# Performance work log

Measured on AMD Instinct MI355X. Metric: run time of the kernel, lower is better.

The kernel has to match this reference:

```python
import jax, jax.numpy as jnp
import numpy as np

N_NODES = 10000
N_EDGES = 160000
T_STEPS = 2
N_SAMPLE = 2
H_DIM = 64
Z_DIM = 32
K_HEADS = 4
N_IN = 4


def setup_inputs() -> dict:
    key = jax.random.key(0)
    ks = jax.random.split(key, 16)
    sc = lambda fan_in: 1.0 / np.sqrt(fan_in).astype(np.float32)
    inp = {}
    inp["inputs"] = jax.random.normal(ks[0], (N_NODES, T_STEPS, N_IN), jnp.float32)
    inp["zA"] = jax.random.normal(ks[1], (N_NODES, N_SAMPLE, Z_DIM), jnp.float32)
    inp["zG"] = jax.random.normal(ks[2], (N_NODES, N_SAMPLE, Z_DIM), jnp.float32)
    inp["src"] = jax.random.randint(ks[3], (N_EDGES,), 0, N_NODES)
    inp["dst"] = jax.random.randint(ks[4], (N_EDGES,), 0, N_NODES)
    # GAT attention projections (K heads, no bias): Linear(z_dim -> h_dim)
    inp["Ws"] = jax.random.normal(ks[5], (K_HEADS, H_DIM, Z_DIM), jnp.float32) * sc(Z_DIM)
    inp["Wd"] = jax.random.normal(ks[6], (K_HEADS, H_DIM, Z_DIM), jnp.float32) * sc(Z_DIM)
    # F2: Linear(2h -> h, no bias), ReLU, Linear(h -> h, no bias)
    inp["F2_w1"] = jax.random.normal(ks[7], (H_DIM, 2 * H_DIM), jnp.float32) * sc(2 * H_DIM)
    inp["F2_w2"] = jax.random.normal(ks[8], (H_DIM, H_DIM), jnp.float32) * sc(H_DIM)
    # F1: Linear(K*h -> h, no bias), ReLU, Linear(h -> h, no bias)
    inp["F1_w1"] = jax.random.normal(ks[9], (H_DIM, K_HEADS * H_DIM), jnp.float32) * sc(K_HEADS * H_DIM)
    inp["F1_w2"] = jax.random.normal(ks[10], (H_DIM, H_DIM), jnp.float32) * sc(H_DIM)
    # x_enc: Linear(n_in -> h) with bias
    inp["xenc_w"] = jax.random.normal(ks[11], (H_DIM, N_IN), jnp.float32) * sc(N_IN)
    inp["xenc_b"] = jnp.zeros((H_DIM,), jnp.float32)
    # out_fc: Linear(h+z -> h), ReLU, Linear(h -> 4)
    inp["out_w1"] = jax.random.normal(ks[12], (H_DIM, H_DIM + Z_DIM), jnp.float32) * sc(H_DIM + Z_DIM)
    inp["out_b1"] = jnp.zeros((H_DIM,), jnp.float32)
    inp["out_w2"] = jax.random.normal(ks[13], (4, H_DIM), jnp.float32) * sc(H_DIM)
    inp["out_b2"] = jnp.zeros((4,), jnp.float32)
    inp["pred_steps"] = 2
    return inp


def reference(inputs, zA, zG, src, dst, Ws, Wd, F2_w1, F2_w2, F1_w1, F1_w2,
              xenc_w, xenc_b, out_w1, out_b1, out_w2, out_b2, pred_steps):
    N, T, _ = inputs.shape
    S = zA.shape[1]
    K = Ws.shape[0]

    # --- edge attention (GAT.attn), computed once per forward ---
    As = jnp.einsum('nsz,khz->nskh', zG, Ws)          # [N, S, K, H]
    Ad = jnp.einsum('nsz,khz->nskh', zG, Wd)
    e = jnp.sum(As[src] * Ad[dst], axis=-1)           # [E, S, K]
    e = jax.nn.leaky_relu(e, 0.01)
    # per-destination softmax over incoming edges (DGL mailbox softmax over dim=1)
    m = jax.ops.segment_max(e, dst, num_segments=N)
    ex = jnp.exp(e - m[dst])
    denom = jax.ops.segment_sum(ex, dst, num_segments=N)
    alpha = ex / denom[dst]                           # [E, S, K]
    deg = jax.ops.segment_sum(jnp.ones((e.shape[0],), e.dtype), dst, num_segments=N)
    deg = jnp.maximum(deg, 1.0)[:, None, None]        # [N, 1, 1]; mean over mailbox dim

    def step(xt):
        xt_enc = xt @ xenc_w.T + xenc_b               # [N, S, H]
        cat = jnp.concatenate([xt_enc[src], xt_enc[dst]], axis=-1)  # [E, S, 2H]
        dA = jax.nn.relu(cat @ F2_w1.T) @ F2_w2.T     # [E, S, H]
        # per-head attention-weighted mean over in-neighbors; loop over K (small, fixed)
        res = [jax.ops.segment_sum(alpha[:, :, k:k + 1] * dA, dst, num_segments=N) / deg
               for k in range(K)]
        res = jnp.concatenate(res, axis=-1)           # [N, S, K*H]
        deltax = jax.nn.relu(res @ F1_w1.T) @ F1_w2.T # [N, S, H]
        h = jnp.concatenate([deltax, zA], axis=-1)    # [N, S, H+Z]
        dx = jax.nn.relu(h @ out_w1.T + out_b1) @ out_w2.T + out_b2  # [N, S, 4]
        return xt + dx

    inp_t = jnp.transpose(inputs, (1, 0, 2))          # [T, N, n_in]
    inp_t = jnp.broadcast_to(inp_t[:, :, None, :], (T, N, S, inp_t.shape[-1]))
    preds = []
    for b in range(0, T, pred_steps):                 # blocks of pred_steps
        xt = inp_t[b]
        for _ in range(pred_steps):
            xt = step(xt)
            preds.append(xt)
    out = jnp.stack(preds, axis=0)                    # [T, N, S, 4]
    return jnp.transpose(out, (1, 0, 2, 3))           # [N, T, S, 4]
```

## Files before the change

### kernel.cpp

```cpp
#include <hip/hip_runtime.h>

#define NN 10000
#define NE 160000
#define TT 2
#define SS 2
#define HH 64
#define ZZ 32
#define KK 4
#define NIN 4

typedef short bf16x8 __attribute__((ext_vector_type(8)));
typedef float f32x4 __attribute__((ext_vector_type(4)));

__device__ __forceinline__ unsigned short f2b(float x) {
    unsigned u = __float_as_uint(x);
    u += 0x7fffu + ((u >> 16) & 1u);
    return (unsigned short)(u >> 16);
}
__device__ __forceinline__ float bf2f(unsigned short u) {
    return __uint_as_float(((unsigned)u) << 16);
}

__device__ __forceinline__ float edge_score(const unsigned* __restrict__ zp,
                                            const float* __restrict__ qf) {
    float a = 0.f;
#pragma unroll
    for (int j = 0; j < 16; ++j) {
        unsigned u = zp[j];
        a += __uint_as_float(u << 16) * qf[2*j]
           + __uint_as_float(u & 0xffff0000u) * qf[2*j+1];
    }
    return a > 0.f ? a : 0.01f*a;
}

__global__ __launch_bounds__(256) void k_prep(
    const float* __restrict__ Ws, const float* __restrict__ Wd,
    const float* __restrict__ F2w1, const float* __restrict__ xw,
    const float* __restrict__ xb, const float* __restrict__ F2w2,
    const float* __restrict__ F1w1, const float* __restrict__ F1w2,
    const float* __restrict__ ow1, const float* __restrict__ ow2,
    const float* __restrict__ zA, const float* __restrict__ zG,
    const float* __restrict__ inputs, const int* __restrict__ dst,
    float* __restrict__ MT, float* __restrict__ G1, float* __restrict__ G2,
    float* __restrict__ c1, float* __restrict__ c2,
    unsigned short* __restrict__ W2b, unsigned short* __restrict__ F1w1b,
    unsigned short* __restrict__ F1w2b, unsigned short* __restrict__ ow1b,
    unsigned short* __restrict__ ow2b, unsigned short* __restrict__ zAb,
    unsigned short* __restrict__ zGb, float* __restrict__ xt,
    int* __restrict__ deg_i)
{
    int b = blockIdx.x;
    int tid = threadIdx.x;
    if (b < 16) {
        int o = b*256 + tid;
        int j = o & 31, i = (o >> 5) & 31, k = o >> 10;
        float acc = 0.0f;
        for (int h = 0; h < HH; ++h)
            acc += Ws[(k*HH + h)*ZZ + i] * Wd[(k*HH + h)*ZZ + j];
        MT[(k*ZZ + j)*ZZ + i] = acc;
    } else if (b == 16) {
        int h = tid >> 2, i = tid & 3;
        float a1 = 0.f, a2 = 0.f;
        for (int j = 0; j < HH; ++j) {
            float x = xw[j*NIN + i];
            a1 += F2w1[h*128 + j] * x;
            a2 += F2w1[h*128 + 64 + j] * x;
        }
        G1[h*4 + i] = a1;
        G2[h*4 + i] = a2;
        if (i == 0) {
            float b1 = 0.f, b2 = 0.f;
            for (int j = 0; j < HH; ++j) {
                float bb = xb[j];
                b1 += F2w1[h*128 + j] * bb;
                b2 += F2w1[h*128 + 64 + j] * bb;
            }
            c1[h] = b1; c2[h] = b2;
        }
    } else {
        int t = (b - 17)*256 + tid;
        if (t < NN*SS*ZZ) { zAb[t] = f2b(zA[t]); zGb[t] = f2b(zG[t]); }
        if (t < HH*HH)    { W2b[t] = f2b(F2w2[t]); F1w2b[t] = f2b(F1w2[t]); }
        if (t < HH*KK*HH) F1w1b[t] = f2b(F1w1[t]);
        if (t < HH*(HH+ZZ)) ow1b[t] = f2b(ow1[t]);
        if (t < 4*HH)     ow2b[t] = f2b(ow2[t]);
        if (t < NN*SS*NIN) {
            int i = t & 3;
            int n = t >> 3;
            xt[t] = inputs[n*(TT*NIN) + i];
        }
        if (t < NE) atomicAdd(deg_i + dst[t], 1);
    }
}

__global__ void k_scan(const int* __restrict__ deg_i, int* __restrict__ offsets,
                       int* __restrict__ cursor) {
    __shared__ int buf0[1024], buf1[1024];
    int tidx = threadIdx.x;
    const int CH = (NN + 1023) / 1024;
    int b0 = tidx * CH;
    int sum = 0;
    for (int i = 0; i < CH; ++i) { int idx = b0 + i; if (idx < NN) sum += deg_i[idx]; }
    buf0[tidx] = sum;
    __syncthreads();
    int* s = buf0; int* d = buf1;
    for (int off = 1; off < 1024; off <<= 1) {
        d[tidx] = s[tidx] + (tidx >= off ? s[tidx - off] : 0);
        __syncthreads();
        int* tmp = s; s = d; d = tmp;
    }
    int run = s[tidx] - sum;
    for (int i = 0; i < CH; ++i) {
        int idx = b0 + i;
        if (idx < NN) { offsets[idx] = run; cursor[idx] = run; run += deg_i[idx]; }
    }
    if (tidx == 0) offsets[NN] = NE;
}

__global__ void k_scatter(const int* __restrict__ src, const int* __restrict__ dst,
                          int* __restrict__ cursor, int* __restrict__ src_by_pos) {
    int e = blockIdx.x * blockDim.x + threadIdx.x;
    if (e >= NE) return;
    int pos = atomicAdd(cursor + dst[e], 1);
    src_by_pos[pos] = src[e];
}

__global__ __launch_bounds__(64) void k_attn_agg0(
    const float* __restrict__ MT, const float* __restrict__ zG,
    const unsigned short* __restrict__ zGb, const int* __restrict__ src_by_pos,
    const int* __restrict__ offsets, const float* __restrict__ xt,
    const float* __restrict__ G1, const float* __restrict__ G2,
    const float* __restrict__ c1, const float* __restrict__ c2,
    float* alpha, unsigned short* __restrict__ agg_b)
{
    __shared__ float sq[128];
    __shared__ float alpha_s[64][4];
    int item = blockIdx.x;
    int n = item >> 1, s = item & 1;
    int l = threadIdx.x;
    int i = l >> 2, k = l & 3;
    int r0 = offsets[n], r1 = offsets[n+1];

    {
        int i0 = l & 31;
        int k0 = l >> 5;
        int k1 = k0 + 2;
        const float* zg = zG + item*ZZ;
        float acc0 = 0.f, acc1 = 0.f;
#pragma unroll
        for (int j = 0; j < ZZ; ++j) {
            float z = zg[j];
            acc0 += MT[(k0*ZZ + j)*ZZ + i0] * z;
            acc1 += MT[(k1*ZZ + j)*ZZ + i0] * z;
        }
        sq[k0*ZZ + i0] = acc0;
        sq[k1*ZZ + i0] = acc1;
    }
    __syncthreads();
    float qf[32];
#pragma unroll
    for (int j = 0; j < 32; ++j) qf[j] = sq[k*ZZ + j];

    float E[8];
    float mx = -1e30f;
    int nit = 0;
    for (int idx = r0 + i; idx < r1; idx += 16, ++nit) {
        int sn = src_by_pos[idx];
        float e = edge_score((const unsigned*)(zGb + (sn*SS + s)*ZZ), qf);
        if (nit < 8) E[nit] = e;
        mx = fmaxf(mx, e);
    }
#pragma unroll
    for (int off = 4; off < 64; off <<= 1) mx = fmaxf(mx, __shfl_xor(mx, off));
    float sum = 0.f;
    nit = 0;
    for (int idx = r0 + i; idx < r1; idx += 16, ++nit) {
        float e = (nit < 8) ? E[nit]
                : edge_score((const unsigned*)(zGb + (src_by_pos[idx]*SS + s)*ZZ), qf);
        sum += __expf(e - mx);
    }
#pragma unroll
    for (int off = 4; off < 64; off <<= 1) sum += __shfl_xor(sum, off);
    int deg = r1 - r0;
    float dd = (float)(deg > 1 ? deg : 1);
    float inv = sum > 0.f ? 1.f/(sum*dd) : 0.f;
    nit = 0;
    for (int idx = r0 + i; idx < r1; idx += 16, ++nit) {
        float e = (nit < 8) ? E[nit]
                : edge_score((const unsigned*)(zGb + (src_by_pos[idx]*SS + s)*ZZ), qf);
        float a = __expf(e - mx) * inv;
        alpha[(idx*2 + s)*4 + k] = a;
        int jo = idx - r0;
        if (jo < 64) alpha_s[jo][k] = a;
    }
    __syncthreads();

    int h = l;
    const float4 g1 = *(const float4*)(G1 + h*4);
    const float4 g2 = *(const float4*)(G2 + h*4);
    const float4 xd = *(const float4*)(xt + item*4);
    float p2 = c2[h] + xd.x*g2.x + xd.y*g2.y + xd.z*g2.z + xd.w*g2.w;
    float c1h = c1[h];
    float a0 = 0.f, a1 = 0.f, a2 = 0.f, a3 = 0.f;
    int jo = 0;
    for (; jo + 4 <= deg; jo += 4) {
        int sn0 = src_by_pos[r0 + jo];
        int sn1 = src_by_pos[r0 + jo + 1];
        int sn2 = src_by_pos[r0 + jo + 2];
        int sn3 = src_by_pos[r0 + jo + 3];
        float4 x0 = *(const float4*)(xt + (sn0*SS + s)*NIN);
        float4 x1 = *(const float4*)(xt + (sn1*SS + s)*NIN);
        float4 x2 = *(const float4*)(xt + (sn2*SS + s)*NIN);
        float4 x3 = *(const float4*)(xt + (sn3*SS + s)*NIN);
        float4 w0 = (jo+0 < 64) ? *(const float4*)(&alpha_s[jo+0][0])
                                : *(const float4*)(alpha + ((r0+jo+0)*2 + s)*4);
        float4 w1 = (jo+1 < 64) ? *(const float4*)(&alpha_s[jo+1][0])
                                : *(const float4*)(alpha + ((r0+jo+1)*2 + s)*4);
        float4 w2 = (jo+2 < 64) ? *(const float4*)(&alpha_s[jo+2][0])
                                : *(const float4*)(alpha + ((r0+jo+2)*2 + s)*4);
        float4 w3 = (jo+3 < 64) ? *(const float4*)(&alpha_s[jo+3][0])
                                : *(const float4*)(alpha + ((r0+jo+3)*2 + s)*4);
        float p, hd;
        p = c1h + x0.x*g1.x + x0.y*g1.y + x0.z*g1.z + x0.w*g1.w;
        hd = p + p2; hd = hd > 0.f ? hd : 0.f;
        a0 += w0.x*hd; a1 += w0.y*hd; a2 += w0.z*hd; a3 += w0.w*hd;
        p = c1h + x1.x*g1.x + x1.y*g1.y + x1.z*g1.z + x1.w*g1.w;
        hd = p + p2; hd = hd > 0.f ? hd : 0.f;
        a0 += w1.x*hd; a1 += w1.y*hd; a2 += w1.z*hd; a3 += w1.w*hd;
        p = c1h + x2.x*g1.x + x2.y*g1.y + x2.z*g1.z + x2.w*g1.w;
        hd = p + p2; hd = hd > 0.f ? hd : 0.f;
        a0 += w2.x*hd; a1 += w2.y*hd; a2 += w2.z*hd; a3 += w2.w*hd;
        p = c1h + x3.x*g1.x + x3.y*g1.y + x3.z*g1.z + x3.w*g1.w;
        hd = p + p2; hd = hd > 0.f ? hd : 0.f;
        a0 += w3.x*hd; a1 += w3.y*hd; a2 += w3.z*hd; a3 += w3.w*hd;
    }
    for (; jo < deg; ++jo) {
        int sn = src_by_pos[r0 + jo];
        float4 x0 = *(const float4*)(xt + (sn*SS + s)*NIN);
        float4 w4 = (jo < 64) ? *(const float4*)(&alpha_s[jo][0])
                              : *(const float4*)(alpha + ((r0+jo)*2 + s)*4);
        float p = c1h + x0.x*g1.x + x0.y*g1.y + x0.z*g1.z + x0.w*g1.w;
        float hd = p + p2; hd = hd > 0.f ? hd : 0.f;
        a0 += w4.x*hd; a1 += w4.y*hd; a2 += w4.z*hd; a3 += w4.w*hd;
    }
    agg_b[item*256 +       h] = f2b(a0);
    agg_b[item*256 + 64  + h] = f2b(a1);
    agg_b[item*256 + 128 + h] = f2b(a2);
    agg_b[item*256 + 192 + h] = f2b(a3);
}

__global__ __launch_bounds__(64) void k_agg2(
    const float* __restrict__ xt, const float* __restrict__ G1,
    const float* __restrict__ G2, const float* __restrict__ c1,
    const float* __restrict__ c2, const int* __restrict__ src_by_pos,
    const int* __restrict__ offsets, const float* __restrict__ alpha,
    unsigned short* __restrict__ agg_b)
{
    int item = blockIdx.x;
    int n = item >> 1, s = item & 1;
    int h = threadIdx.x;
    int r0 = offsets[n], r1 = offsets[n+1];
    const float4 g1 = *(const float4*)(G1 + h*4);
    const float4 g2 = *(const float4*)(G2 + h*4);
    const float4 xd = *(const float4*)(xt + item*4);
    float p2 = c2[h] + xd.x*g2.x + xd.y*g2.y + xd.z*g2.z + xd.w*g2.w;
    float c1h = c1[h];
    float a0 = 0.f, a1 = 0.f, a2 = 0.f, a3 = 0.f;
    int idx = r0;
    for (; idx + 4 <= r1; idx += 4) {
        int sn0 = src_by_pos[idx];
        int sn1 = src_by_pos[idx+1];
        int sn2 = src_by_pos[idx+2];
        int sn3 = src_by_pos[idx+3];
        float4 x0 = *(const float4*)(xt + (sn0*SS + s)*NIN);
        float4 x1 = *(const float4*)(xt + (sn1*SS + s)*NIN);
        float4 x2 = *(const float4*)(xt + (sn2*SS + s)*NIN);
        float4 x3 = *(const float4*)(xt + (sn3*SS + s)*NIN);
        float4 w0 = *(const float4*)(alpha + ((idx+0)*2 + s)*4);
        float4 w1 = *(const float4*)(alpha + ((idx+1)*2 + s)*4);
        float4 w2 = *(const float4*)(alpha + ((idx+2)*2 + s)*4);
        float4 w3 = *(const float4*)(alpha + ((idx+3)*2 + s)*4);
        float p, hd;
        p = c1h + x0.x*g1.x + x0.y*g1.y + x0.z*g1.z + x0.w*g1.w;
        hd = p + p2; hd = hd > 0.f ? hd : 0.f;
        a0 += w0.x*hd; a1 += w0.y*hd; a2 += w0.z*hd; a3 += w0.w*hd;
        p = c1h + x1.x*g1.x + x1.y*g1.y + x1.z*g1.z + x1.w*g1.w;
        hd = p + p2; hd = hd > 0.f ? hd : 0.f;
        a0 += w1.x*hd; a1 += w1.y*hd; a2 += w1.z*hd; a3 += w1.w*hd;
        p = c1h + x2.x*g1.x + x2.y*g1.y + x2.z*g1.z + x2.w*g1.w;
        hd = p + p2; hd = hd > 0.f ? hd : 0.f;
        a0 += w2.x*hd; a1 += w2.y*hd; a2 += w2.z*hd; a3 += w2.w*hd;
        p = c1h + x3.x*g1.x + x3.y*g1.y + x3.z*g1.z + x3.w*g1.w;
        hd = p + p2; hd = hd > 0.f ? hd : 0.f;
        a0 += w3.x*hd; a1 += w3.y*hd; a2 += w3.z*hd; a3 += w3.w*hd;
    }
    for (; idx < r1; ++idx) {
        int sn = src_by_pos[idx];
        float4 x0 = *(const float4*)(xt + (sn*SS + s)*NIN);
        float4 w0 = *(const float4*)(alpha + (idx*2 + s)*4);
        float p = c1h + x0.x*g1.x + x0.y*g1.y + x0.z*g1.z + x0.w*g1.w;
        float hd = p + p2; hd = hd > 0.f ? hd : 0.f;
        a0 += w0.x*hd; a1 += w0.y*hd; a2 += w0.z*hd; a3 += w0.w*hd;
    }
    agg_b[item*256 +       h] = f2b(a0);
    agg_b[item*256 + 64  + h] = f2b(a1);
    agg_b[item*256 + 128 + h] = f2b(a2);
    agg_b[item*256 + 192 + h] = f2b(a3);
}

__global__ __launch_bounds__(256) void k_node_mfma(
    const unsigned short* __restrict__ agg_b, const unsigned short* __restrict__ zAb,
    const unsigned short* __restrict__ W2b,
    const unsigned short* __restrict__ F1w1b, const unsigned short* __restrict__ F1w2b,
    const unsigned short* __restrict__ ow1b, const unsigned short* __restrict__ ow2b,
    const float* __restrict__ ob1, const float* __restrict__ ob2,
    float* __restrict__ xt, float* __restrict__ out, int tstep)
{
    __shared__ unsigned short res_s[4][16*264];
    __shared__ unsigned short hid_s[4][16*72];
    __shared__ unsigned short hcat_s[4][16*104];
    int tid = threadIdx.x;
    int w = tid >> 6, l = tid & 63, l15 = l & 15, qq = l >> 4;

    bf16x8 w2f[2][4], b2f[2][4], o1f[3][4], bo2[2];
#pragma unroll
    for (int nb = 0; nb < 4; ++nb) {
        int n = nb*16 + l15;
#pragma unroll
        for (int kb = 0; kb < 2; ++kb) {
            w2f[kb][nb] = *(const bf16x8*)(W2b  + n*64 + kb*32 + qq*8);
            b2f[kb][nb] = *(const bf16x8*)(F1w2b + n*64 + kb*32 + qq*8);
        }
#pragma unroll
        for (int kb = 0; kb < 3; ++kb)
            o1f[kb][nb] = *(const bf16x8*)(ow1b + n*96 + kb*32 + qq*8);
    }
#pragma unroll
    for (int kb = 0; kb < 2; ++kb) {
        if (l15 < 4) bo2[kb] = *(const bf16x8*)(ow2b + l15*64 + kb*32 + qq*8);
        else {
            bf16x8 z;
#pragma unroll
            for (int j = 0; j < 8; ++j) z[j] = 0;
            bo2[kb] = z;
        }
    }
    float b1v[4];
#pragma unroll
    for (int nb = 0; nb < 4; ++nb) b1v[nb] = ob1[nb*16 + l15];
    float b2v = (l15 < 4) ? ob2[l15] : 0.0f;

    int itemBase = blockIdx.x*64 + w*16;
    if (itemBase >= NN*SS) return;

    *(uint4*)(&hcat_s[w][l15*104 + 64 + qq*8]) =
        *(const uint4*)(zAb + (itemBase + l15)*ZZ + qq*8);

#pragma unroll
    for (int k = 0; k < 4; ++k) {
        f32x4 acc0[4];
#pragma unroll
        for (int nb = 0; nb < 4; ++nb) acc0[nb] = (f32x4)(0.0f);
#pragma unroll
        for (int kb = 0; kb < 2; ++kb) {
            bf16x8 af = *(const bf16x8*)(agg_b + (itemBase + l15)*256 + k*64 + kb*32 + qq*8);
#pragma unroll
            for (int nb = 0; nb < 4; ++nb)
                acc0[nb] = __builtin_amdgcn_mfma_f32_16x16x32_bf16(af, w2f[kb][nb], acc0[nb], 0, 0, 0);
        }
#pragma unroll
        for (int nb = 0; nb < 4; ++nb)
#pragma unroll
            for (int r = 0; r < 4; ++r)
                res_s[w][(qq*4 + r)*264 + k*64 + nb*16 + l15] = f2b(acc0[nb][r]);
    }

    f32x4 acc[4];
#pragma unroll
    for (int nb = 0; nb < 4; ++nb) acc[nb] = (f32x4)(0.0f);
#pragma unroll
    for (int kb = 0; kb < 8; ++kb) {
        bf16x8 af = *(const bf16x8*)(&res_s[w][l15*264 + kb*32 + qq*8]);
#pragma unroll
        for (int nb = 0; nb < 4; ++nb) {
            bf16x8 bf = *(const bf16x8*)(F1w1b + (nb*16 + l15)*256 + kb*32 + qq*8);
            acc[nb] = __builtin_amdgcn_mfma_f32_16x16x32_bf16(af, bf, acc[nb], 0, 0, 0);
        }
    }
#pragma unroll
    for (int nb = 0; nb < 4; ++nb)
#pragma unroll
        for (int r = 0; r < 4; ++r) {
            float v = acc[nb][r];
            hid_s[w][(qq*4 + r)*72 + nb*16 + l15] = f2b(v > 0.0f ? v : 0.0f);
        }

    f32x4 acc2[4];
#pragma unroll
    for (int nb = 0; nb < 4; ++nb) acc2[nb] = (f32x4)(0.0f);
#pragma unroll
    for (int kb = 0; kb < 2; ++kb) {
        bf16x8 af = *(const bf16x8*)(&hid_s[w][l15*72 + kb*32 + qq*8]);
#pragma unroll
        for (int nb = 0; nb < 4; ++nb)
            acc2[nb] = __builtin_amdgcn_mfma_f32_16x16x32_bf16(af, b2f[kb][nb], acc2[nb], 0, 0, 0);
    }
#pragma unroll
    for (int nb = 0; nb < 4; ++nb)
#pragma unroll
        for (int r = 0; r < 4; ++r)
            hcat_s[w][(qq*4 + r)*104 + nb*16 + l15] = f2b(acc2[nb][r]);

    f32x4 acc3[4];
#pragma unroll
    for (int nb = 0; nb < 4; ++nb) acc3[nb] = (f32x4)(0.0f);
#pragma unroll
    for (int kb = 0; kb < 3; ++kb) {
        bf16x8 af = *(const bf16x8*)(&hcat_s[w][l15*104 + kb*32 + qq*8]);
#pragma unroll
        for (int nb = 0; nb < 4; ++nb)
            acc3[nb] = __builtin_amdgcn_mfma_f32_16x16x32_bf16(af, o1f[kb][nb], acc3[nb], 0, 0, 0);
    }
#pragma unroll
    for (int nb = 0; nb < 4; ++nb)
#pragma unroll
        for (int r = 0; r < 4; ++r) {
            float v = acc3[nb][r] + b1v[nb];
            hid_s[w][(qq*4 + r)*72 + nb*16 + l15] = f2b(v > 0.0f ? v : 0.0f);
        }

    f32x4 acc4 = (f32x4)(0.0f);
#pragma unroll
    for (int kb = 0; kb < 2; ++kb) {
        bf16x8 af = *(const bf16x8*)(&hid_s[w][l15*72 + kb*32 + qq*8]);
        acc4 = __builtin_amdgcn_mfma_f32_16x16x32_bf16(af, bo2[kb], acc4, 0, 0, 0);
    }
    if (l15 < 4) {
#pragma unroll
        for (int r = 0; r < 4; ++r) {
            int item = itemBase + qq*4 + r;
            float nx = xt[item*4 + l15] + acc4[r] + b2v;
            xt[item*4 + l15] = nx;
            int n = item >> 1, s = item & 1;
            out[((n*TT + tstep)*SS + s)*4 + l15] = nx;
        }
    }
}

extern "C" void kernel_launch(void* const* d_in, const int* in_sizes, int n_in,
                              void* d_out, int out_size, void* d_ws, size_t ws_size,
                              hipStream_t stream) {
    const float* inputs = (const float*)d_in[0];
    const float* zA     = (const float*)d_in[1];
    const float* zG     = (const float*)d_in[2];
    const int*   src    = (const int*)d_in[3];
    const int*   dst    = (const int*)d_in[4];
    const float* Ws     = (const float*)d_in[5];
    const float* Wd     = (const float*)d_in[6];
    const float* F2w1   = (const float*)d_in[7];
    const float* F2w2   = (const float*)d_in[8];
    const float* F1w1   = (const float*)d_in[9];
    const float* F1w2   = (const float*)d_in[10];
    const float* xw     = (const float*)d_in[11];
    const float* xb     = (const float*)d_in[12];
    const float* ow1    = (const float*)d_in[13];
    const float* ob1    = (const float*)d_in[14];
    const float* ow2    = (const float*)d_in[15];
    const float* ob2    = (const float*)d_in[16];
    float* out = (float*)d_out;

    float*          base        = (float*)d_ws;
    float*          MT          = base;
    float*          alpha       = base + 4096;
    int*            deg_i       = (int*)(base + 1284096);
    int*            offsets     = (int*)(base + 1294096);
    int*            cursor      = (int*)(base + 1304112);
    int*            src_by_pos  = (int*)(base + 1314112);
    float*          xt          = base + 1474112;
    float*          G1f         = base + 1554112;
    float*          G2f         = base + 1554368;
    float*          c1f         = base + 1554624;
    float*          c2f         = base + 1554688;
    unsigned short* W2b         = (unsigned short*)(base + 1554816);
    unsigned short* F1w1b       = (unsigned short*)(base + 1556864);
    unsigned short* F1w2b       = (unsigned short*)(base + 1565056);
    unsigned short* ow1b        = (unsigned short*)(base + 1567104);
    unsigned short* ow2b        = (unsigned short*)(base + 1570176);
    unsigned short* zAb         = (unsigned short*)(base + 1570304);
    unsigned short* zGb         = (unsigned short*)(base + 1890304);
    unsigned short* agg_b       = (unsigned short*)(base + 2210304);

    hipMemsetAsync(deg_i, 0, 10000u * 4u, stream);

    const int CONVB = (NN*SS*ZZ + 255)/256;
    k_prep<<<17 + CONVB, 256, 0, stream>>>(Ws, Wd, F2w1, xw, xb, F2w2, F1w1, F1w2,
                                           ow1, ow2, zA, zG, inputs, dst,
                                           MT, G1f, G2f, c1f, c2f,
                                           W2b, F1w1b, F1w2b, ow1b, ow2b,
                                           zAb, zGb, xt, deg_i);
    k_scan<<<1, 1024, 0, stream>>>(deg_i, offsets, cursor);
    k_scatter<<<(NE + 255)/256, 256, 0, stream>>>(src, dst, cursor, src_by_pos);

    k_attn_agg0<<<NN*SS, 64, 0, stream>>>(MT, zG, zGb, src_by_pos, offsets, xt,
                                          G1f, G2f, c1f, c2f, alpha, agg_b);
    k_node_mfma<<<(NN*SS + 63)/64, 256, 0, stream>>>(agg_b, zAb, W2b, F1w1b, F1w2b,
                                                     ow1b, ow2b, ob1, ob2, xt, out, 0);
    k_agg2<<<NN*SS, 64, 0, stream>>>(xt, G1f, G2f, c1f, c2f,
                                     src_by_pos, offsets, alpha, agg_b);
    k_node_mfma<<<(NN*SS + 63)/64, 256, 0, stream>>>(agg_b, zAb, W2b, F1w1b, F1w2b,
                                                     ow1b, ow2b, ob1, ob2, xt, out, 1);
}
```

Baseline: 225.6 us.

## Precompute per-node source projections and attention queries, pair samples per block

Moves the per-edge source-side projection (c1 + x·G1) into a per-node precomputed buffer u, filled by an extended scan kernel for step 0 and by the node MFMA kernel for step 1. Attention query vectors are likewise precomputed per item in the scan kernel, and edge scores load bf16 rows as 16-byte vectors. The aggregation kernels now process both samples of a node in one 128-thread block and cache exp values instead of recomputing them. The trade is redundant per-edge arithmetic for extra global traffic (reading a 64-float u row per edge) and extra buffers.

```diff
diff --git a/kernel.cpp b/kernel.cpp
--- a/kernel.cpp
+++ b/kernel.cpp
@@ -17,18 +17,24 @@
     u += 0x7fffu + ((u >> 16) & 1u);
     return (unsigned short)(u >> 16);
 }
-__device__ __forceinline__ float bf2f(unsigned short u) {
-    return __uint_as_float(((unsigned)u) << 16);
-}
-
-__device__ __forceinline__ float edge_score(const unsigned* __restrict__ zp,
+
+__device__ __forceinline__ float edge_score(const unsigned short* __restrict__ zrow,
                                             const float* __restrict__ qf) {
+    const uint4* zp = (const uint4*)zrow;
     float a = 0.f;
 #pragma unroll
-    for (int j = 0; j < 16; ++j) {
-        unsigned u = zp[j];
-        a += __uint_as_float(u << 16) * qf[2*j]
-           + __uint_as_float(u & 0xffff0000u) * qf[2*j+1];
+    for (int q = 0; q < 4; ++q) {
+        uint4 v = zp[q];
+        unsigned uu0 = v.x, uu1 = v.y, uu2 = v.z, uu3 = v.w;
+        int j = q * 8;
+        a += __uint_as_float(uu0 << 16)         * qf[j+0]
+           + __uint_as_float(uu0 & 0xffff0000u) * qf[j+1];
+        a += __uint_as_float(uu1 << 16)         * qf[j+2]
+           + __uint_as_float(uu1 & 0xffff0000u) * qf[j+3];
+        a += __uint_as_float(uu2 << 16)         * qf[j+4]
+           + __uint_as_float(uu2 & 0xffff0000u) * qf[j+5];
+        a += __uint_as_float(uu3 << 16)         * qf[j+6]
+           + __uint_as_float(uu3 & 0xffff0000u) * qf[j+7];
     }
     return a > 0.f ? a : 0.01f*a;
 }
@@ -93,28 +99,51 @@
     }
 }
 
-__global__ void k_scan(const int* __restrict__ deg_i, int* __restrict__ offsets,
-                       int* __restrict__ cursor) {
-    __shared__ int buf0[1024], buf1[1024];
-    int tidx = threadIdx.x;
-    const int CH = (NN + 1023) / 1024;
-    int b0 = tidx * CH;
-    int sum = 0;
-    for (int i = 0; i < CH; ++i) { int idx = b0 + i; if (idx < NN) sum += deg_i[idx]; }
-    buf0[tidx] = sum;
-    __syncthreads();
-    int* s = buf0; int* d = buf1;
-    for (int off = 1; off < 1024; off <<= 1) {
-        d[tidx] = s[tidx] + (tidx >= off ? s[tidx - off] : 0);
+__global__ __launch_bounds__(256) void k_scan2(
+    const int* __restrict__ deg_i, int* __restrict__ offsets,
+    int* __restrict__ cursor,
+    const float* __restrict__ MT, const float* __restrict__ zG,
+    const float* __restrict__ xt, const float* __restrict__ G1,
+    const float* __restrict__ c1, float* __restrict__ qd, float* __restrict__ u)
+{
+    int b = blockIdx.x;
+    int tid = threadIdx.x;
+    if (b == 0) {
+        __shared__ int buf0[256], buf1[256];
+        const int CH = (NN + 255) / 256;
+        int b0 = tid * CH;
+        int sum = 0;
+        for (int i = 0; i < CH; ++i) { int idx = b0 + i; if (idx < NN) sum += deg_i[idx]; }
+        buf0[tid] = sum;
         __syncthreads();
-        int* tmp = s; s = d; d = tmp;
-    }
-    int run = s[tidx] - sum;
-    for (int i = 0; i < CH; ++i) {
-        int idx = b0 + i;
-        if (idx < NN) { offsets[idx] = run; cursor[idx] = run; run += deg_i[idx]; }
-    }
-    if (tidx == 0) offsets[NN] = NE;
+        int* s = buf0; int* d = buf1;
+        for (int off = 1; off < 256; off <<= 1) {
+            d[tid] = s[tid] + (tid >= off ? s[tid - off] : 0);
+            __syncthreads();
+            int* tmp = s; s = d; d = tmp;
+        }
+        int run = s[tid] - sum;
+        for (int i = 0; i < CH; ++i) {
+            int idx = b0 + i;
+            if (idx < NN) { offsets[idx] = run; cursor[idx] = run; run += deg_i[idx]; }
+        }
+        if (tid == 0) offsets[NN] = NE;
+    } else if (b <= 10000) {
+        int o = (b - 1)*256 + tid;
+        int i = o & 31, k = (o >> 5) & 3, item = o >> 7;
+        const float* zg = zG + item*ZZ;
+        float acc = 0.f;
+#pragma unroll
+        for (int j = 0; j < ZZ; ++j)
+            acc += MT[(k*ZZ + j)*ZZ + i] * zg[j];
+        qd[o] = acc;
+    } else {
+        int o = (b - 10001)*256 + tid;
+        int h = o & 63, item = o >> 6;
+        float4 g = *(const float4*)(G1 + h*4);
+        float4 x = *(const float4*)(xt + item*4);
+        u[o] = c1[h] + x.x*g.x + x.y*g.y + x.z*g.z + x.w*g.w;
+    }
 }
 
 __global__ void k_scatter(const int* __restrict__ src, const int* __restrict__ dst,
@@ -125,49 +154,40 @@
     src_by_pos[pos] = src[e];
 }
 
-__global__ __launch_bounds__(64) void k_attn_agg0(
-    const float* __restrict__ MT, const float* __restrict__ zG,
-    const unsigned short* __restrict__ zGb, const int* __restrict__ src_by_pos,
-    const int* __restrict__ offsets, const float* __restrict__ xt,
-    const float* __restrict__ G1, const float* __restrict__ G2,
-    const float* __restrict__ c1, const float* __restrict__ c2,
-    float* alpha, unsigned short* __restrict__ agg_b)
+__global__ __launch_bounds__(128) void k_attn_agg0(
+    const float* __restrict__ qd, const unsigned short* __restrict__ zGb,
+    const int* __restrict__ src_by_pos, const int* __restrict__ offsets,
+    const float* __restrict__ xt, const float* __restrict__ u,
+    const float* __restrict__ G2, const float* __restrict__ c2,
+    float* __restrict__ alpha, unsigned short* __restrict__ agg_b)
 {
-    __shared__ float sq[128];
-    __shared__ float alpha_s[64][4];
-    int item = blockIdx.x;
-    int n = item >> 1, s = item & 1;
-    int l = threadIdx.x;
+    __shared__ float alpha_s[2][64][4];
+    int n = blockIdx.x;
+    int tid = threadIdx.x;
+    int s = tid >> 6;
+    int l = tid & 63;
     int i = l >> 2, k = l & 3;
+    int item = n*2 + s;
     int r0 = offsets[n], r1 = offsets[n+1];
-
+    int deg = r1 - r0;
+
+    float qf[32];
     {
-        int i0 = l & 31;
-        int k0 = l >> 5;
-        int k1 = k0 + 2;
-        const float* zg = zG + item*ZZ;
-        float acc0 = 0.f, acc1 = 0.f;
-#pragma unroll
-        for (int j = 0; j < ZZ; ++j) {
-            float z = zg[j];
-            acc0 += MT[(k0*ZZ + j)*ZZ + i0] * z;
-            acc1 += MT[(k1*ZZ + j)*ZZ + i0] * z;
-        }
-        sq[k0*ZZ + i0] = acc0;
-        sq[k1*ZZ + i0] = acc1;
-    }
-    __syncthreads();
-    float qf[32];
-#pragma unroll
-    for (int j = 0; j < 32; ++j) qf[j] = sq[k*ZZ + j];
-
-    float E[8];
+        const float4* qp = (const float4*)(qd + item*128 + k*32);
+#pragma unroll
+        for (int j = 0; j < 8; ++j) {
+            float4 v = qp[j];
+            qf[4*j] = v.x; qf[4*j+1] = v.y; qf[4*j+2] = v.z; qf[4*j+3] = v.w;
+        }
+    }
+
+    float E[6];
     float mx = -1e30f;
     int nit = 0;
     for (int idx = r0 + i; idx < r1; idx += 16, ++nit) {
         int sn = src_by_pos[idx];
-        float e = edge_score((const unsigned*)(zGb + (sn*SS + s)*ZZ), qf);
-        if (nit < 8) E[nit] = e;
+        float e = edge_score(zGb + (sn*SS + s)*ZZ, qf);
+        if (nit < 6) E[nit] = e;
         mx = fmaxf(mx, e);
     }
 #pragma unroll
@@ -175,32 +195,31 @@
     float sum = 0.f;
     nit = 0;
     for (int idx = r0 + i; idx < r1; idx += 16, ++nit) {
-        float e = (nit < 8) ? E[nit]
-                : edge_score((const unsigned*)(zGb + (src_by_pos[idx]*SS + s)*ZZ), qf);
-        sum += __expf(e - mx);
+        float e = (nit < 6) ? E[nit]
+                : edge_score(zGb + (src_by_pos[idx]*SS + s)*ZZ, qf);
+        float ex = __expf(e - mx);
+        if (nit < 6) E[nit] = ex;
+        sum += ex;
     }
 #pragma unroll
     for (int off = 4; off < 64; off <<= 1) sum += __shfl_xor(sum, off);
-    int deg = r1 - r0;
     float dd = (float)(deg > 1 ? deg : 1);
     float inv = sum > 0.f ? 1.f/(sum*dd) : 0.f;
     nit = 0;
     for (int idx = r0 + i; idx < r1; idx += 16, ++nit) {
-        float e = (nit < 8) ? E[nit]
-                : edge_score((const unsigned*)(zGb + (src_by_pos[idx]*SS + s)*ZZ), qf);
-        float a = __expf(e - mx) * inv;
+        float a = ((nit < 6) ? E[nit]
+                 : __expf(edge_score(zGb + (src_by_pos[idx]*SS + s)*ZZ, qf) - mx)) * inv;
         alpha[(idx*2 + s)*4 + k] = a;
         int jo = idx - r0;
-        if (jo < 64) alpha_s[jo][k] = a;
+        if (jo < 64) alpha_s[s][jo][k] = a;
     }
     __syncthreads();
 
     int h = l;
-    const float4 g1 = *(const float4*)(G1 + h*4);
-    const float4 g2 = *(const float4*)(G2 + h*4);
+    const float4 g2v = *(const float4*)(G2 + h*4);
     const float4 xd = *(const float4*)(xt + item*4);
-    float p2 = c2[h] + xd.x*g2.x + xd.y*g2.y + xd.z*g2.z + xd.w*g2.w;
-    float c1h = c1[h];
+    float p2 = c2[h] + xd.x*g2v.x + xd.y*g2v.y + xd.z*g2v.z + xd.w*g2v.w;
+    const float* ub = u + s*64 + h;
     float a0 = 0.f, a1 = 0.f, a2 = 0.f, a3 = 0.f;
     int jo = 0;
     for (; jo + 4 <= deg; jo += 4) {
@@ -208,39 +227,34 @@
         int sn1 = src_by_pos[r0 + jo + 1];
         int sn2 = src_by_pos[r0 + jo + 2];
         int sn3 = src_by_pos[r0 + jo + 3];
-        float4 x0 = *(const float4*)(xt + (sn0*SS + s)*NIN);
-        float4 x1 = *(const float4*)(xt + (sn1*SS + s)*NIN);
-        float4 x2 = *(const float4*)(xt + (sn2*SS + s)*NIN);
-        float4 x3 = *(const float4*)(xt + (sn3*SS + s)*NIN);
-        float4 w0 = (jo+0 < 64) ? *(const float4*)(&alpha_s[jo+0][0])
+        float us0 = ub[sn0*128];
+        float us1 = ub[sn1*128];
+        float us2 = ub[sn2*128];
+        float us3 = ub[sn3*128];
+        float4 w0 = (jo+0 < 64) ? *(const float4*)(&alpha_s[s][jo+0][0])
                                 : *(const float4*)(alpha + ((r0+jo+0)*2 + s)*4);
-        float4 w1 = (jo+1 < 64) ? *(const float4*)(&alpha_s[jo+1][0])
+        float4 w1 = (jo+1 < 64) ? *(const float4*)(&alpha_s[s][jo+1][0])
                                 : *(const float4*)(alpha + ((r0+jo+1)*2 + s)*4);
-        float4 w2 = (jo+2 < 64) ? *(const float4*)(&alpha_s[jo+2][0])
+        float4 w2 = (jo+2 < 64) ? *(const float4*)(&alpha_s[s][jo+2][0])
                                 : *(const float4*)(alpha + ((r0+jo+2)*2 + s)*4);
-        float4 w3 = (jo+3 < 64) ? *(const float4*)(&alpha_s[jo+3][0])
+        float4 w3 = (jo+3 < 64) ? *(const float4*)(&alpha_s[s][jo+3][0])
                                 : *(const float4*)(alpha + ((r0+jo+3)*2 + s)*4);
-        float p, hd;
-        p = c1h + x0.x*g1.x + x0.y*g1.y + x0.z*g1.z + x0.w*g1.w;
-        hd = p + p2; hd = hd > 0.f ? hd : 0.f;
+        float hd;
+        hd = us0 + p2; hd = hd > 0.f ? hd : 0.f;
         a0 += w0.x*hd; a1 += w0.y*hd; a2 += w0.z*hd; a3 += w0.w*hd;
-        p = c1h + x1.x*g1.x + x1.y*g1.y + x1.z*g1.z + x1.w*g1.w;
-        hd = p + p2; hd = hd > 0.f ? hd : 0.f;
+        hd = us1 + p2; hd = hd > 0.f ? hd : 0.f;
         a0 += w1.x*hd; a1 += w1.y*hd; a2 += w1.z*hd; a3 += w1.w*hd;
-        p = c1h + x2.x*g1.x + x2.y*g1.y + x2.z*g1.z + x2.w*g1.w;
-        hd = p + p2; hd = hd > 0.f ? hd : 0.f;
+        hd = us2 + p2; hd = hd > 0.f ? hd : 0.f;
         a0 += w2.x*hd; a1 += w2.y*hd; a2 += w2.z*hd; a3 += w2.w*hd;
-        p = c1h + x3.x*g1.x + x3.y*g1.y + x3.z*g1.z + x3.w*g1.w;
-        hd = p + p2; hd = hd > 0.f ? hd : 0.f;
+        hd = us3 + p2; hd = hd > 0.f ? hd : 0.f;
         a0 += w3.x*hd; a1 += w3.y*hd; a2 += w3.z*hd; a3 += w3.w*hd;
     }
     for (; jo < deg; ++jo) {
         int sn = src_by_pos[r0 + jo];
-        float4 x0 = *(const float4*)(xt + (sn*SS + s)*NIN);
-        float4 w4 = (jo < 64) ? *(const float4*)(&alpha_s[jo][0])
+        float us = ub[sn*128];
+        float4 w4 = (jo < 64) ? *(const float4*)(&alpha_s[s][jo][0])
                               : *(const float4*)(alpha + ((r0+jo)*2 + s)*4);
-        float p = c1h + x0.x*g1.x + x0.y*g1.y + x0.z*g1.z + x0.w*g1.w;
-        float hd = p + p2; hd = hd > 0.f ? hd : 0.f;
+        float hd = us + p2; hd = hd > 0.f ? hd : 0.f;
         a0 += w4.x*hd; a1 += w4.y*hd; a2 += w4.z*hd; a3 += w4.w*hd;
     }
     agg_b[item*256 +       h] = f2b(a0);
@@ -249,22 +263,21 @@
     agg_b[item*256 + 192 + h] = f2b(a3);
 }
 
-__global__ __launch_bounds__(64) void k_agg2(
-    const float* __restrict__ xt, const float* __restrict__ G1,
-    const float* __restrict__ G2, const float* __restrict__ c1,
-    const float* __restrict__ c2, const int* __restrict__ src_by_pos,
-    const int* __restrict__ offsets, const float* __restrict__ alpha,
-    unsigned short* __restrict__ agg_b)
+__global__ __launch_bounds__(128) void k_agg2(
+    const float* __restrict__ xt, const float* __restrict__ u,
+    const float* __restrict__ G2, const float* __restrict__ c2,
+    const int* __restrict__ src_by_pos, const int* __restrict__ offsets,
+    const float* __restrict__ alpha, unsigned short* __restrict__ agg_b)
 {
-    int item = blockIdx.x;
-    int n = item >> 1, s = item & 1;
-    int h = threadIdx.x;
+    int n = blockIdx.x;
+    int tid = threadIdx.x;
+    int s = tid >> 6, h = tid & 63;
+    int item = n*2 + s;
     int r0 = offsets[n], r1 = offsets[n+1];
-    const float4 g1 = *(const float4*)(G1 + h*4);
-    const float4 g2 = *(const float4*)(G2 + h*4);
+    const float4 g2v = *(const float4*)(G2 + h*4);
     const float4 xd = *(const float4*)(xt + item*4);
-    float p2 = c2[h] + xd.x*g2.x + xd.y*g2.y + xd.z*g2.z + xd.w*g2.w;
-    float c1h = c1[h];
+    float p2 = c2[h] + xd.x*g2v.x + xd.y*g2v.y + xd.z*g2v.z + xd.w*g2v.w;
+    const float* ub = u + s*64 + h;
     float a0 = 0.f, a1 = 0.f, a2 = 0.f, a3 = 0.f;
     int idx = r0;
     for (; idx + 4 <= r1; idx += 4) {
@@ -272,34 +285,29 @@
         int sn1 = src_by_pos[idx+1];
         int sn2 = src_by_pos[idx+2];
         int sn3 = src_by_pos[idx+3];
-        float4 x0 = *(const float4*)(xt + (sn0*SS + s)*NIN);
-        float4 x1 = *(const float4*)(xt + (sn1*SS + s)*NIN);
-        float4 x2 = *(const float4*)(xt + (sn2*SS + s)*NIN);
-        float4 x3 = *(const float4*)(xt + (sn3*SS + s)*NIN);
+        float us0 = ub[sn0*128];
+        float us1 = ub[sn1*128];
+        float us2 = ub[sn2*128];
+        float us3 = ub[sn3*128];
         float4 w0 = *(const float4*)(alpha + ((idx+0)*2 + s)*4);
         float4 w1 = *(const float4*)(alpha + ((idx+1)*2 + s)*4);
         float4 w2 = *(const float4*)(alpha + ((idx+2)*2 + s)*4);
         float4 w3 = *(const float4*)(alpha + ((idx+3)*2 + s)*4);
-        float p, hd;
-        p = c1h + x0.x*g1.x + x0.y*g1.y + x0.z*g1.z + x0.w*g1.w;
-        hd = p + p2; hd = hd > 0.f ? hd : 0.f;
+        float hd;
+        hd = us0 + p2; hd = hd > 0.f ? hd : 0.f;
         a0 += w0.x*hd; a1 += w0.y*hd; a2 += w0.z*hd; a3 += w0.w*hd;
-        p = c1h + x1.x*g1.x + x1.y*g1.y + x1.z*g1.z + x1.w*g1.w;
-        hd = p + p2; hd = hd > 0.f ? hd : 0.f;
+        hd = us1 + p2; hd = hd > 0.f ? hd : 0.f;
         a0 += w1.x*hd; a1 += w1.y*hd; a2 += w1.z*hd; a3 += w1.w*hd;
-        p = c1h + x2.x*g1.x + x2.y*g1.y + x2.z*g1.z + x2.w*g1.w;
-        hd = p + p2; hd = hd > 0.f ? hd : 0.f;
+        hd = us2 + p2; hd = hd > 0.f ? hd : 0.f;
         a0 += w2.x*hd; a1 += w2.y*hd; a2 += w2.z*hd; a3 += w2.w*hd;
-        p = c1h + x3.x*g1.x + x3.y*g1.y + x3.z*g1.z + x3.w*g1.w;
-        hd = p + p2; hd = hd > 0.f ? hd : 0.f;
+        hd = us3 + p2; hd = hd > 0.f ? hd : 0.f;
         a0 += w3.x*hd; a1 += w3.y*hd; a2 += w3.z*hd; a3 += w3.w*hd;
     }
     for (; idx < r1; ++idx) {
         int sn = src_by_pos[idx];
-        float4 x0 = *(const float4*)(xt + (sn*SS + s)*NIN);
+        float us = ub[sn*128];
         float4 w0 = *(const float4*)(alpha + (idx*2 + s)*4);
-        float p = c1h + x0.x*g1.x + x0.y*g1.y + x0.z*g1.z + x0.w*g1.w;
-        float hd = p + p2; hd = hd > 0.f ? hd : 0.f;
+        float hd = us + p2; hd = hd > 0.f ? hd : 0.f;
         a0 += w0.x*hd; a1 += w0.y*hd; a2 += w0.z*hd; a3 += w0.w*hd;
     }
     agg_b[item*256 +       h] = f2b(a0);
@@ -314,11 +322,14 @@
     const unsigned short* __restrict__ F1w1b, const unsigned short* __restrict__ F1w2b,
     const unsigned short* __restrict__ ow1b, const unsigned short* __restrict__ ow2b,
     const float* __restrict__ ob1, const float* __restrict__ ob2,
+    const float* __restrict__ G1, const float* __restrict__ c1,
+    float* __restrict__ u,
     float* __restrict__ xt, float* __restrict__ out, int tstep)
 {
     __shared__ unsigned short res_s[4][16*264];
     __shared__ unsigned short hid_s[4][16*72];
     __shared__ unsigned short hcat_s[4][16*104];
+    __shared__ float xs[4][16][4];
     int tid = threadIdx.x;
     int w = tid >> 6, l = tid & 63, l15 = l & 15, qq = l >> 4;
 
@@ -441,8 +452,20 @@
             int item = itemBase + qq*4 + r;
             float nx = xt[item*4 + l15] + acc4[r] + b2v;
             xt[item*4 + l15] = nx;
+            xs[w][qq*4 + r][l15] = nx;
             int n = item >> 1, s = item & 1;
             out[((n*TT + tstep)*SS + s)*4 + l15] = nx;
+        }
+    }
+    if (tstep == 0) {
+        asm volatile("s_waitcnt lgkmcnt(0)" ::: "memory");
+        float4 g1v = *(const float4*)(G1 + l*4);
+        float c1v = c1[l];
+#pragma unroll
+        for (int it = 0; it < 16; ++it) {
+            float4 xv = *(const float4*)(&xs[w][it][0]);
+            u[(itemBase + it)*64 + l] =
+                c1v + xv.x*g1v.x + xv.y*g1v.y + xv.z*g1v.z + xv.w*g1v.w;
         }
     }
 }
@@ -489,6 +512,8 @@
     unsigned short* zAb         = (unsigned short*)(base + 1570304);
     unsigned short* zGb         = (unsigned short*)(base + 1890304);
     unsigned short* agg_b       = (unsigned short*)(base + 2210304);
+    float*          qd          = base + 4770304;
+    float*          u           = base + 7330304;
 
     hipMemsetAsync(deg_i, 0, 10000u * 4u, stream);
 
@@ -498,15 +523,18 @@
                                            MT, G1f, G2f, c1f, c2f,
                                            W2b, F1w1b, F1w2b, ow1b, ow2b,
                                            zAb, zGb, xt, deg_i);
-    k_scan<<<1, 1024, 0, stream>>>(deg_i, offsets, cursor);
+    k_scan2<<<15001, 256, 0, stream>>>(deg_i, offsets, cursor,
+                                       MT, zG, xt, G1f, c1f, qd, u);
     k_scatter<<<(NE + 255)/256, 256, 0, stream>>>(src, dst, cursor, src_by_pos);
 
-    k_attn_agg0<<<NN*SS, 64, 0, stream>>>(MT, zG, zGb, src_by_pos, offsets, xt,
-                                          G1f, G2f, c1f, c2f, alpha, agg_b);
+    k_attn_agg0<<<NN, 128, 0, stream>>>(qd, zGb, src_by_pos, offsets, xt, u,
+                                        G2f, c2f, alpha, agg_b);
     k_node_mfma<<<(NN*SS + 63)/64, 256, 0, stream>>>(agg_b, zAb, W2b, F1w1b, F1w2b,
-                                                     ow1b, ow2b, ob1, ob2, xt, out, 0);
-    k_agg2<<<NN*SS, 64, 0, stream>>>(xt, G1f, G2f, c1f, c2f,
-                                     src_by_pos, offsets, alpha, agg_b);
+                                                     ow1b, ow2b, ob1, ob2,
+                                                     G1f, c1f, u, xt, out, 0);
+    k_agg2<<<NN, 128, 0, stream>>>(xt, u, G2f, c2f,
+                                   src_by_pos, offsets, alpha, agg_b);
     k_node_mfma<<<(NN*SS + 63)/64, 256, 0, stream>>>(agg_b, zAb, W2b, F1w1b, F1w2b,
-                                                     ow1b, ow2b, ob1, ob2, xt, out, 1);
-}
+                                                     ow1b, ow2b, ob1, ob2,
+                                                     G1f, c1f, u, xt, out, 1);
+}
```

Measured after the change: 254.0 us. 12.6% more time.

## Precompute per-node attention queries in scan kernel and cache exp values

Applied to the files above, without the earlier changes.

Moves the per-item query projection (MT x zG) out of the attention kernel into extra blocks of the scan kernel, which now runs as a 256-thread scan plus 10000 parallel query blocks. The query work then overlaps the serial scan, and the attention kernel loses a syncthreads and its shared scratch. The edge-score loads are widened to 16-byte uint4 reads, and cached exponentials avoid recomputing expf in the final pass. In exchange the kernel writes and reads a 10 MB qd buffer through global memory, and the single-block scan now uses fewer threads.

```diff
diff --git a/kernel.cpp b/kernel.cpp
--- a/kernel.cpp
+++ b/kernel.cpp
@@ -17,18 +17,24 @@
     u += 0x7fffu + ((u >> 16) & 1u);
     return (unsigned short)(u >> 16);
 }
-__device__ __forceinline__ float bf2f(unsigned short u) {
-    return __uint_as_float(((unsigned)u) << 16);
-}
-
-__device__ __forceinline__ float edge_score(const unsigned* __restrict__ zp,
+
+__device__ __forceinline__ float edge_score(const unsigned short* __restrict__ zrow,
                                             const float* __restrict__ qf) {
+    const uint4* zp = (const uint4*)zrow;
     float a = 0.f;
 #pragma unroll
-    for (int j = 0; j < 16; ++j) {
-        unsigned u = zp[j];
-        a += __uint_as_float(u << 16) * qf[2*j]
-           + __uint_as_float(u & 0xffff0000u) * qf[2*j+1];
+    for (int q = 0; q < 4; ++q) {
+        uint4 v = zp[q];
+        unsigned uu0 = v.x, uu1 = v.y, uu2 = v.z, uu3 = v.w;
+        int j = q * 8;
+        a += __uint_as_float(uu0 << 16)         * qf[j+0]
+           + __uint_as_float(uu0 & 0xffff0000u) * qf[j+1];
+        a += __uint_as_float(uu1 << 16)         * qf[j+2]
+           + __uint_as_float(uu1 & 0xffff0000u) * qf[j+3];
+        a += __uint_as_float(uu2 << 16)         * qf[j+4]
+           + __uint_as_float(uu2 & 0xffff0000u) * qf[j+5];
+        a += __uint_as_float(uu3 << 16)         * qf[j+6]
+           + __uint_as_float(uu3 & 0xffff0000u) * qf[j+7];
     }
     return a > 0.f ? a : 0.01f*a;
 }
@@ -93,28 +99,44 @@
     }
 }
 
-__global__ void k_scan(const int* __restrict__ deg_i, int* __restrict__ offsets,
-                       int* __restrict__ cursor) {
-    __shared__ int buf0[1024], buf1[1024];
-    int tidx = threadIdx.x;
-    const int CH = (NN + 1023) / 1024;
-    int b0 = tidx * CH;
-    int sum = 0;
-    for (int i = 0; i < CH; ++i) { int idx = b0 + i; if (idx < NN) sum += deg_i[idx]; }
-    buf0[tidx] = sum;
-    __syncthreads();
-    int* s = buf0; int* d = buf1;
-    for (int off = 1; off < 1024; off <<= 1) {
-        d[tidx] = s[tidx] + (tidx >= off ? s[tidx - off] : 0);
+__global__ __launch_bounds__(256) void k_scan2(
+    const int* __restrict__ deg_i, int* __restrict__ offsets,
+    int* __restrict__ cursor,
+    const float* __restrict__ MT, const float* __restrict__ zG,
+    float* __restrict__ qd)
+{
+    int b = blockIdx.x;
+    int tid = threadIdx.x;
+    if (b == 0) {
+        __shared__ int buf0[256], buf1[256];
+        const int CH = (NN + 255) / 256;
+        int b0 = tid * CH;
+        int sum = 0;
+        for (int i = 0; i < CH; ++i) { int idx = b0 + i; if (idx < NN) sum += deg_i[idx]; }
+        buf0[tid] = sum;
         __syncthreads();
-        int* tmp = s; s = d; d = tmp;
-    }
-    int run = s[tidx] - sum;
-    for (int i = 0; i < CH; ++i) {
-        int idx = b0 + i;
-        if (idx < NN) { offsets[idx] = run; cursor[idx] = run; run += deg_i[idx]; }
-    }
-    if (tidx == 0) offsets[NN] = NE;
+        int* s = buf0; int* d = buf1;
+        for (int off = 1; off < 256; off <<= 1) {
+            d[tid] = s[tid] + (tid >= off ? s[tid - off] : 0);
+            __syncthreads();
+            int* tmp = s; s = d; d = tmp;
+        }
+        int run = s[tid] - sum;
+        for (int i = 0; i < CH; ++i) {
+            int idx = b0 + i;
+            if (idx < NN) { offsets[idx] = run; cursor[idx] = run; run += deg_i[idx]; }
+        }
+        if (tid == 0) offsets[NN] = NE;
+    } else {
+        int o = (b - 1)*256 + tid;
+        int i = o & 31, k = (o >> 5) & 3, item = o >> 7;
+        const float* zg = zG + item*ZZ;
+        float acc = 0.f;
+#pragma unroll
+        for (int j = 0; j < ZZ; ++j)
+            acc += MT[(k*ZZ + j)*ZZ + i] * zg[j];
+        qd[o] = acc;
+    }
 }
 
 __global__ void k_scatter(const int* __restrict__ src, const int* __restrict__ dst,
@@ -126,47 +148,37 @@
 }
 
 __global__ __launch_bounds__(64) void k_attn_agg0(
-    const float* __restrict__ MT, const float* __restrict__ zG,
-    const unsigned short* __restrict__ zGb, const int* __restrict__ src_by_pos,
-    const int* __restrict__ offsets, const float* __restrict__ xt,
+    const float* __restrict__ qd, const unsigned short* __restrict__ zGb,
+    const int* __restrict__ src_by_pos, const int* __restrict__ offsets,
+    const float* __restrict__ xt,
     const float* __restrict__ G1, const float* __restrict__ G2,
     const float* __restrict__ c1, const float* __restrict__ c2,
-    float* alpha, unsigned short* __restrict__ agg_b)
+    float* __restrict__ alpha, unsigned short* __restrict__ agg_b)
 {
-    __shared__ float sq[128];
     __shared__ float alpha_s[64][4];
     int item = blockIdx.x;
     int n = item >> 1, s = item & 1;
     int l = threadIdx.x;
     int i = l >> 2, k = l & 3;
     int r0 = offsets[n], r1 = offsets[n+1];
-
+    int deg = r1 - r0;
+
+    float qf[32];
     {
-        int i0 = l & 31;
-        int k0 = l >> 5;
-        int k1 = k0 + 2;
-        const float* zg = zG + item*ZZ;
-        float acc0 = 0.f, acc1 = 0.f;
-#pragma unroll
-        for (int j = 0; j < ZZ; ++j) {
-            float z = zg[j];
-            acc0 += MT[(k0*ZZ + j)*ZZ + i0] * z;
-            acc1 += MT[(k1*ZZ + j)*ZZ + i0] * z;
-        }
-        sq[k0*ZZ + i0] = acc0;
-        sq[k1*ZZ + i0] = acc1;
-    }
-    __syncthreads();
-    float qf[32];
-#pragma unroll
-    for (int j = 0; j < 32; ++j) qf[j] = sq[k*ZZ + j];
+        const float4* qp = (const float4*)(qd + item*128 + k*32);
+#pragma unroll
+        for (int j = 0; j < 8; ++j) {
+            float4 v = qp[j];
+            qf[4*j] = v.x; qf[4*j+1] = v.y; qf[4*j+2] = v.z; qf[4*j+3] = v.w;
+        }
+    }
 
     float E[8];
     float mx = -1e30f;
     int nit = 0;
     for (int idx = r0 + i; idx < r1; idx += 16, ++nit) {
         int sn = src_by_pos[idx];
-        float e = edge_score((const unsigned*)(zGb + (sn*SS + s)*ZZ), qf);
+        float e = edge_score(zGb + (sn*SS + s)*ZZ, qf);
         if (nit < 8) E[nit] = e;
         mx = fmaxf(mx, e);
     }
@@ -176,19 +188,19 @@
     nit = 0;
     for (int idx = r0 + i; idx < r1; idx += 16, ++nit) {
         float e = (nit < 8) ? E[nit]
-                : edge_score((const unsigned*)(zGb + (src_by_pos[idx]*SS + s)*ZZ), qf);
-        sum += __expf(e - mx);
+                : edge_score(zGb + (src_by_pos[idx]*SS + s)*ZZ, qf);
+        float ex = __expf(e - mx);
+        if (nit < 8) E[nit] = ex;
+        sum += ex;
     }
 #pragma unroll
     for (int off = 4; off < 64; off <<= 1) sum += __shfl_xor(sum, off);
-    int deg = r1 - r0;
     float dd = (float)(deg > 1 ? deg : 1);
     float inv = sum > 0.f ? 1.f/(sum*dd) : 0.f;
     nit = 0;
     for (int idx = r0 + i; idx < r1; idx += 16, ++nit) {
-        float e = (nit < 8) ? E[nit]
-                : edge_score((const unsigned*)(zGb + (src_by_pos[idx]*SS + s)*ZZ), qf);
-        float a = __expf(e - mx) * inv;
+        float a = ((nit < 8) ? E[nit]
+                 : __expf(edge_score(zGb + (src_by_pos[idx]*SS + s)*ZZ, qf) - mx)) * inv;
         alpha[(idx*2 + s)*4 + k] = a;
         int jo = idx - r0;
         if (jo < 64) alpha_s[jo][k] = a;
@@ -489,6 +501,7 @@
     unsigned short* zAb         = (unsigned short*)(base + 1570304);
     unsigned short* zGb         = (unsigned short*)(base + 1890304);
     unsigned short* agg_b       = (unsigned short*)(base + 2210304);
+    float*          qd          = base + 4770304;
 
     hipMemsetAsync(deg_i, 0, 10000u * 4u, stream);
 
@@ -498,10 +511,10 @@
                                            MT, G1f, G2f, c1f, c2f,
                                            W2b, F1w1b, F1w2b, ow1b, ow2b,
                                            zAb, zGb, xt, deg_i);
-    k_scan<<<1, 1024, 0, stream>>>(deg_i, offsets, cursor);
+    k_scan2<<<10001, 256, 0, stream>>>(deg_i, offsets, cursor, MT, zG, qd);
     k_scatter<<<(NE + 255)/256, 256, 0, stream>>>(src, dst, cursor, src_by_pos);
 
-    k_attn_agg0<<<NN*SS, 64, 0, stream>>>(MT, zG, zGb, src_by_pos, offsets, xt,
+    k_attn_agg0<<<NN*SS, 64, 0, stream>>>(qd, zGb, src_by_pos, offsets, xt,
                                           G1f, G2f, c1f, c2f, alpha, agg_b);
     k_node_mfma<<<(NN*SS + 63)/64, 256, 0, stream>>>(agg_b, zAb, W2b, F1w1b, F1w2b,
                                                      ow1b, ow2b, ob1, ob2, xt, out, 0);
```

After: 258.0 us. 1.14x slower.
